# Performance work log

Measured on AMD Instinct MI355X. Metric: run time of the kernel, lower is better.

Reference implementation:

```python
import jax, jax.numpy as jnp
import numpy as np

B, T, V, D, H, A = 256, 512, 50000, 256, 256, 128


def setup_inputs() -> dict:
    key = jax.random.key(0)
    ks = jax.random.split(key, 9)
    x = jax.random.randint(ks[0], (B, T), 0, V, dtype=jnp.int32)
    embed_w = jax.random.uniform(ks[1], (V, D), dtype=jnp.float32)          # random_uniform init, non-trainable
    lstm_kernel = jax.random.normal(ks[2], (D + H, 4 * H), dtype=jnp.float32) * 0.05  # BasicLSTMCell kernel [i,j,f,o]
    lstm_bias = jnp.zeros((4 * H,), jnp.float32)
    w_omega = jax.random.normal(ks[3], (H, A), dtype=jnp.float32)
    b_omega = jax.random.normal(ks[4], (A,), dtype=jnp.float32)
    u_omega = jax.random.normal(ks[5], (A,), dtype=jnp.float32)
    w = jax.random.normal(ks[6], (H, 2), dtype=jnp.float32)
    b = jnp.zeros((2,), jnp.float32)
    return {"x": x, "embed_w": embed_w, "lstm_kernel": lstm_kernel,
            "lstm_bias": lstm_bias, "w_omega": w_omega, "b_omega": b_omega,
            "u_omega": u_omega, "w": w, "b": b}


def _lstm_attention_forward(x, embed_w, lstm_kernel, lstm_bias, w_omega, b_omega, u_omega, w, b):
    Bt, Tt = x.shape
    Hh = lstm_bias.shape[0] // 4
    seq_len = jnp.sum(jnp.sign(x), axis=1)                         # [B] like tf.reduce_sum(tf.sign(x))
    e = embed_w[x]                                                  # [B,T,D] embedding lookup
    # dynamic_rnn semantics: outputs zeroed past seq_len, state frozen
    mask = (jnp.arange(Tt)[:, None] < seq_len[None, :]).astype(e.dtype)  # [T,B]
    xs = (jnp.transpose(e, (1, 0, 2)), mask[:, :, None])            # time-major

    def step(carry, inp):
        c, h = carry
        x_t, m = inp                                                # [B,D], [B,1]
        z = jnp.concatenate([x_t, h], axis=-1) @ lstm_kernel + lstm_bias  # [B,4H]
        i, j, f, o = jnp.split(z, 4, axis=-1)
        c_new = c * jax.nn.sigmoid(f + 1.0) + jax.nn.sigmoid(i) * jnp.tanh(j)  # forget_bias=1.0
        h_new = jnp.tanh(c_new) * jax.nn.sigmoid(o)
        c = jnp.where(m > 0, c_new, c)
        h_out = h_new * m
        h = jnp.where(m > 0, h_new, h)
        return (c, h), h_out

    c0 = jnp.zeros((Bt, Hh), e.dtype)
    h0 = jnp.zeros((Bt, Hh), e.dtype)
    _, outs = jax.lax.scan(step, (c0, h0), xs)                      # [T,B,H]
    outs = jnp.transpose(outs, (1, 0, 2))                           # [B,T,H]

    # additive attention pooling
    value = jnp.tanh(jnp.einsum('bth,ha->bta', outs, w_omega) + b_omega)
    vu = jnp.einsum('bta,a->bt', value, u_omega)
    alphas = jax.nn.softmax(vu, axis=-1)                            # [B,T]
    last = jnp.sum(outs * alphas[..., None], axis=1)                # [B,H]

    logits = last @ w + b                                           # [B,2]
    return jax.nn.softmax(logits)


def reference(x, embed_w, lstm_kernel, lstm_bias, w_omega, b_omega, u_omega, w, b):
    return _lstm_attention_forward(x, embed_w, lstm_kernel, lstm_bias,
                                   w_omega, b_omega, u_omega, w, b)
```

## Files before the change

### kernel.cpp

```cpp
#include <hip/hip_runtime.h>
#include <hip/hip_bf16.h>
#include <cstdint>
#include <cstddef>

typedef _Float16 f16;
typedef _Float16 f16x8 __attribute__((ext_vector_type(8)));
typedef _Float16 f16x4 __attribute__((ext_vector_type(4)));
typedef float f32x4 __attribute__((ext_vector_type(4)));
typedef unsigned long long u64;
typedef unsigned int u32;

#define B_   256
#define T_   512
#define V_   50000
#define D_   256
#define H_   256
#define A_   128
#define N4H  1024

__device__ __forceinline__ float sigmoid_f(float x) {
    return __builtin_amdgcn_rcpf(1.f + __expf(-x));
}
__device__ __forceinline__ float tanh_f(float x) {
    float e = __expf(-2.f * fabsf(x));
    float t = 1.f - 2.f * e * __builtin_amdgcn_rcpf(1.f + e);
    return copysignf(t, x);
}

#define MFMA_A(accv, afragv, bfraga)                                         \
    asm volatile("v_mfma_f32_16x16x32_f16 %0, %1, %2, %0"                    \
                 : "+v"(accv) : "v"(afragv), "a"(bfraga))

#define LGKM_BARRIER()                                                       \
    do {                                                                     \
        asm volatile("s_waitcnt lgkmcnt(0)" ::: "memory");                   \
        __builtin_amdgcn_sched_barrier(0);                                   \
        __builtin_amdgcn_s_barrier();                                        \
        __builtin_amdgcn_sched_barrier(0);                                   \
    } while (0)

__global__ __launch_bounds__(256) void k0_convert(
    const float* __restrict__ lstm_kernel, const float* __restrict__ w_omega,
    f16* __restrict__ WxT, f16* __restrict__ WhT, f16* __restrict__ WomT) {
    int blk = blockIdx.x;
    int tau = threadIdx.x;
    if (blk < N4H) {
        int n = blk;
        WxT[n * 256 + tau] = (f16)lstm_kernel[(size_t)tau * N4H + n];
        WhT[n * 256 + tau] = (f16)lstm_kernel[(size_t)(256 + tau) * N4H + n];
    } else {
        int a = blk - N4H;
        WomT[a * 256 + tau] = (f16)w_omega[(size_t)tau * A_ + a];
    }
}

__global__ __launch_bounds__(256) void k1_seqlen(
    const int* __restrict__ x, int* __restrict__ seqlen) {
    __shared__ int red[256];
    int b = blockIdx.x, tau = threadIdx.x;
    int cnt = (x[b * T_ + tau] != 0) + (x[b * T_ + tau + 256] != 0);
    red[tau] = cnt;
    __syncthreads();
    for (int s = 128; s > 0; s >>= 1) {
        if (tau < s) red[tau] += red[tau + s];
        __syncthreads();
    }
    if (tau == 0) seqlen[b] = red[0];
}

__global__ __launch_bounds__(256) void k2_zx(
    const int* __restrict__ x, const float* __restrict__ embed,
    const f16* __restrict__ WxT, const float* __restrict__ bias,
    f16* __restrict__ Zx, int t0, int Tc) {
    __shared__ __align__(16) f16 A_s[64][264];
    __shared__ __align__(16) f16 B_s[128][72];
    __shared__ int tok_s[64];

    int tau  = threadIdx.x;
    int bm   = blockIdx.x;
    int i0   = bm * 64;
    int wave = tau >> 6, lane = tau & 63;
    int q = lane >> 4, c = lane & 15;

    if (tau < 64) {
        int i  = i0 + tau;
        int bb = i / Tc, tr = i - bb * Tc;
        tok_s[tau] = x[bb * T_ + t0 + tr];
    }
    __syncthreads();

    {
        int r = tau >> 2, quarter = tau & 3;
        const float4* src =
            (const float4*)(embed + (size_t)tok_s[r] * D_ + quarter * 64);
        f16* dst = &A_s[r][quarter * 64];
#pragma unroll
        for (int j = 0; j < 16; j++) {
            float4 v = src[j];
            dst[j * 4 + 0] = (f16)v.x;
            dst[j * 4 + 1] = (f16)v.y;
            dst[j * 4 + 2] = (f16)v.z;
            dst[j * 4 + 3] = (f16)v.w;
        }
    }

    for (int np = 0; np < 8; np++) {
        f32x4 acc[8];
#pragma unroll
        for (int ni = 0; ni < 8; ni++) acc[ni] = (f32x4){0.f, 0.f, 0.f, 0.f};

        for (int kt = 0; kt < 4; kt++) {
            __syncthreads();
            {
                int n = tau >> 1, half = tau & 1;
                const f16x8* src = (const f16x8*)(WxT +
                    (size_t)(np * 128 + n) * 256 + kt * 64 + half * 32);
                f16x8* dst = (f16x8*)&B_s[n][half * 32];
#pragma unroll
                for (int j = 0; j < 4; j++) dst[j] = src[j];
            }
            __syncthreads();
#pragma unroll
            for (int s = 0; s < 2; s++) {
                f16x8 afrag =
                    *(const f16x8*)&A_s[wave * 16 + c][kt * 64 + s * 32 + q * 8];
#pragma unroll
                for (int ni = 0; ni < 8; ni++) {
                    f16x8 bfrag = *(const f16x8*)&B_s[ni * 16 + c][s * 32 + q * 8];
                    acc[ni] = __builtin_amdgcn_mfma_f32_16x16x32_f16(
                        afrag, bfrag, acc[ni], 0, 0, 0);
                }
            }
        }
#pragma unroll
        for (int ni = 0; ni < 8; ni++) {
            int n    = np * 128 + ni * 16 + c;
            int g    = n >> 8, rem = n & 255;
            int half = rem >> 7, colu = rem & 127;
            int np2  = half * 512 + colu * 4 + g;
            float bv = bias[n];
#pragma unroll
            for (int r = 0; r < 4; r++) {
                int row = i0 + wave * 16 + q * 4 + r;
                Zx[(size_t)row * N4H + np2] = (f16)(acc[ni][r] + bv);
            }
        }
    }
}

#define SMEM_BYTES 87040

__device__ __forceinline__ void zx_producer(
    const int* __restrict__ x, const float* __restrict__ embed,
    const f16* __restrict__ WxT, const float* __restrict__ bias,
    f16* __restrict__ Zx, int pb, int t0, int Tc, char* smem) {
    f16 (*Ap_s)[264] = (f16(*)[264])smem;
    f16 (*Bp_s)[72]  = (f16(*)[72])(smem + 67584);
    int* tokp_s      = (int*)(smem + 86016);

    int tau  = threadIdx.x;
    int i0   = pb * 128;
    int wave = tau >> 6, lane = tau & 63;
    int q = lane >> 4, c = lane & 15;

    if (tau < 128) {
        int i  = i0 + tau;
        int bb = i / Tc, tr = i - bb * Tc;
        tokp_s[tau] = x[bb * T_ + t0 + tr];
    }
    __syncthreads();

    {
        int r = tau >> 2, quarter = tau & 3;
        const float4* src =
            (const float4*)(embed + (size_t)tokp_s[r] * D_ + quarter * 64);
        f16* dst = &Ap_s[r][quarter * 64];
#pragma unroll
        for (int j = 0; j < 16; j++) {
            float4 v = src[j];
            dst[j * 4 + 0] = (f16)v.x;
            dst[j * 4 + 1] = (f16)v.y;
            dst[j * 4 + 2] = (f16)v.z;
            dst[j * 4 + 3] = (f16)v.w;
        }
    }

    for (int np = 0; np < 8; np++) {
        f32x4 acc[8];
#pragma unroll
        for (int ni = 0; ni < 8; ni++) acc[ni] = (f32x4){0.f, 0.f, 0.f, 0.f};

        for (int kt = 0; kt < 4; kt++) {
            __syncthreads();
            {
                int n = tau >> 2, qt = tau & 3;
                const f16x8* src = (const f16x8*)(WxT +
                    (size_t)(np * 128 + n) * 256 + kt * 64 + qt * 16);
                f16x8* dst = (f16x8*)&Bp_s[n][qt * 16];
                dst[0] = src[0];
                dst[1] = src[1];
            }
            __syncthreads();
#pragma unroll
            for (int s = 0; s < 2; s++) {
                f16x8 afrag =
                    *(const f16x8*)&Ap_s[wave * 16 + c][kt * 64 + s * 32 + q * 8];
#pragma unroll
                for (int ni = 0; ni < 8; ni++) {
                    f16x8 bfrag = *(const f16x8*)&Bp_s[ni * 16 + c][s * 32 + q * 8];
                    acc[ni] = __builtin_amdgcn_mfma_f32_16x16x32_f16(
                        afrag, bfrag, acc[ni], 0, 0, 0);
                }
            }
        }
#pragma unroll
        for (int ni = 0; ni < 8; ni++) {
            int n     = np * 128 + ni * 16 + c;
            int g     = n >> 8, rem = n & 255;
            int halfn = rem >> 7, colu = rem & 127;
            int np2   = halfn * 512 + colu * 4 + g;
            float bv  = bias[n];
#pragma unroll
            for (int r = 0; r < 4; r++) {
                int row = i0 + wave * 16 + q * 4 + r;
                Zx[(size_t)row * N4H + np2] = (f16)(acc[ni][r] + bv);
            }
        }
    }
}

__device__ __forceinline__ void vu_producer(
    const f16* __restrict__ outs, const f16* __restrict__ WomT,
    const float* __restrict__ b_omega, const float* __restrict__ u_omega,
    float* __restrict__ vuout, int b, int t0v, int Tc, char* smem) {
    f16 (*A_s)[264]   = (f16(*)[264])smem;
    f16 (*val_s)[132] = (f16(*)[132])(smem + 33792);
    float* u_s        = (float*)(smem + 50688);

    int tau  = threadIdx.x;
    int wave = tau >> 6, lane = tau & 63;
    int q = lane >> 4, c = lane & 15;

    if (tau < 128) u_s[tau] = u_omega[tau];
    float bom[8];
#pragma unroll
    for (int ni = 0; ni < 8; ni++) bom[ni] = b_omega[ni * 16 + c];

    int nchap = Tc >> 6;
    for (int ch = 0; ch < nchap; ch++) {
        int t0c = t0v + ch * 64;
        __syncthreads();
        if (tau < 256) {
            int r = tau >> 2, seg = tau & 3;
            const f16x8* src =
                (const f16x8*)(outs + ((size_t)b * T_ + t0c + r) * H_ + seg * 64);
            f16x8* dst = (f16x8*)&A_s[r][seg * 64];
#pragma unroll
            for (int j = 0; j < 8; j++) dst[j] = src[j];
        }
        __syncthreads();
        if (tau < 256) {
            f32x4 acc[8];
#pragma unroll
            for (int ni = 0; ni < 8; ni++) acc[ni] = (f32x4){0.f, 0.f, 0.f, 0.f};
#pragma unroll
            for (int kc = 0; kc < 8; kc++) {
                f16x8 afrag = *(const f16x8*)&A_s[wave * 16 + c][kc * 32 + q * 8];
#pragma unroll
                for (int ni = 0; ni < 8; ni++) {
                    f16x8 bfrag = *(const f16x8*)(WomT +
                        (size_t)(ni * 16 + c) * 256 + kc * 32 + q * 8);
                    acc[ni] = __builtin_amdgcn_mfma_f32_16x16x32_f16(
                        afrag, bfrag, acc[ni], 0, 0, 0);
                }
            }
#pragma unroll
            for (int ni = 0; ni < 8; ni++) {
#pragma unroll
                for (int r = 0; r < 4; r++) {
                    val_s[wave * 16 + q * 4 + r][ni * 16 + c] =
                        (f16)tanh_f(acc[ni][r] + bom[ni]);
                }
            }
        }
        __syncthreads();
        if (tau < 64) {
            float s = 0.f;
#pragma unroll 8
            for (int a = 0; a < 128; a++) s += (float)val_s[tau][a] * u_s[a];
            vuout[(size_t)b * T_ + t0c + tau] = s;
        }
    }
}

__global__ __launch_bounds__(512, 2) void k3_lstm(
    const f16* __restrict__ Zx, const f16* __restrict__ WhT,
    const int* __restrict__ seqlen, f16* __restrict__ outs,
    f16* __restrict__ Hstate, float* __restrict__ Cstate,
    u32* __restrict__ Hex, int t0, int Tc, int first, int last,
    const int* __restrict__ x, const float* __restrict__ embed,
    const f16* __restrict__ WxT, const float* __restrict__ bias,
    f16* __restrict__ ZxNext, int t0n, int npz,
    const f16* __restrict__ WomT, const float* __restrict__ b_omega,
    const float* __restrict__ u_omega, float* __restrict__ vuout, int t0v) {
    __shared__ __align__(16) char smem[SMEM_BYTES];

    if (blockIdx.x >= 32) {
        int pid = blockIdx.x - 32;
        if (pid < npz)
            zx_producer(x, embed, WxT, bias, ZxNext, pid, t0n, Tc, smem);
        else
            vu_producer(outs, WomT, b_omega, u_omega, vuout, pid - npz, t0v,
                        Tc, smem);
        return;
    }

    f16 (*Zx_s)[16][520] = (f16(*)[16][520])smem;
    f16 (*h_s)[16][264]  = (f16(*)[16][264])(smem + 33280);

    int tau  = threadIdx.x;
    int w    = tau >> 6, lane = tau & 63;
    int q = lane >> 4, c = lane & 15;
    int wgid = blockIdx.x;
    int pair = wgid >> 1, half = wgid & 1;
    int b0 = pair * 16;
    int u0 = half * 128, pu0 = (half ^ 1) * 128;
    int u  = u0 + w * 16 + c;
    int col = w * 16 + c;

    u32* hexw_my = Hex + (size_t)wgid * 2 * 2048;
    u32* hexw_pr = Hex + (size_t)(wgid ^ 1) * 2 * 2048;

    f32x4 wha[4][8];
#pragma unroll
    for (int g = 0; g < 4; g++)
#pragma unroll
        for (int s = 0; s < 8; s++) {
            int kc = (s < 4) ? (half * 4 + s) : ((half ^ 1) * 4 + (s - 4));
            f16x8 f = *(const f16x8*)(WhT +
                (size_t)(g * 256 + u0 + w * 16 + c) * 256 + kc * 32 + q * 8);
            f32x4 t = __builtin_bit_cast(f32x4, f);
            asm volatile("" : "=a"(wha[g][s]) : "0"(t));
        }

    int kOwn = half * 128 + q * 8;
    int kPar = (half ^ 1) * 128 + q * 8;

    int p0 = t0 & 1;
    if (first) {
        for (int idx = tau; idx < 2 * 16 * 264; idx += 512)
            ((f16*)h_s)[idx] = (f16)0.f;
    } else {
        for (int idx = tau; idx < 16 * 256; idx += 512) {
            int r = idx >> 8, k = idx & 255;
            h_s[p0][r][k] = Hstate[(b0 + r) * H_ + k];
        }
    }

    float cst[4];
    f16   hprev[4];
    int   sl[4];
#pragma unroll
    for (int r = 0; r < 4; r++) {
        int row = q * 4 + r;
        cst[r]   = first ? 0.f : Cstate[(b0 + row) * H_ + u];
        hprev[r] = first ? (f16)0.f : Hstate[(b0 + row) * H_ + u];
        sl[r]    = seqlen[b0 + row];
    }

    int r_st = tau >> 5;
    int cc   = (tau & 31) * 16;
    const f16* zxrow = Zx + ((size_t)(b0 + r_st) * Tc) * N4H + half * 512 + cc;

    {
        const f16x8* src = (const f16x8*)zxrow;
        f16x8* dst = (f16x8*)&Zx_s[p0][r_st][cc];
        dst[0] = src[0];
        dst[1] = src[1];
    }
    int rr = tau >> 5;
    int uu = (tau & 31) * 4;

    __syncthreads();

    f32x4 accO[4];
#pragma unroll
    for (int g = 0; g < 4; g++) accO[g] = (f32x4){0.f, 0.f, 0.f, 0.f};
#pragma unroll
    for (int kk = 0; kk < 4; kk++) {
        f16x8 afrag = *(const f16x8*)&h_s[p0][c][kOwn + kk * 32];
#pragma unroll
        for (int g = 0; g < 4; g++) MFMA_A(accO[g], afrag, wha[g][kk]);
    }

    u64 vp0 = 0, vp1 = 0;

    for (int tt = 0; tt < Tc; tt++) {
        int t   = t0 + tt;
        int cur = t & 1, nxt = cur ^ 1;

        int tn = (tt + 1 < Tc) ? tt + 1 : tt;
        const f16x8* psrc = (const f16x8*)(zxrow + (size_t)tn * N4H);
        f16x8 z0 = psrc[0];
        f16x8 z1 = psrc[1];

        if (tt > 0) {
            u32 tagp = (u32)(t & 0xffff);
            const u64* pp = (const u64*)&hexw_pr[cur * 2048 + rr * 128 + uu];
            while (((u32)(vp0 >> 16) & 0xffffu) != tagp ||
                   ((u32)(vp0 >> 48)) != tagp ||
                   ((u32)(vp1 >> 16) & 0xffffu) != tagp ||
                   ((u32)(vp1 >> 48)) != tagp) {
                vp0 = __hip_atomic_load(pp + 0, __ATOMIC_RELAXED,
                                        __HIP_MEMORY_SCOPE_AGENT);
                vp1 = __hip_atomic_load(pp + 1, __ATOMIC_RELAXED,
                                        __HIP_MEMORY_SCOPE_AGENT);
            }
            u64 hw = (u64)(vp0 & 0xffff) | (((vp0 >> 32) & 0xffff) << 16) |
                     ((vp1 & 0xffff) << 32) | (((vp1 >> 32) & 0xffff) << 48);
            *(u64*)&h_s[cur][rr][pu0 + uu] = hw;
        }
        LGKM_BARRIER();

#pragma unroll
        for (int kk = 0; kk < 4; kk++) {
            f16x8 afrag = *(const f16x8*)&h_s[cur][c][kPar + kk * 32];
#pragma unroll
            for (int g = 0; g < 4; g++) MFMA_A(accO[g], afrag, wha[g][4 + kk]);
        }

        u32 tag = (u32)((t + 1) & 0xffff);
        f16 ovals[4];
#pragma unroll
        for (int r = 0; r < 4; r++) {
            int row = q * 4 + r;
            f16x4 zv = *(const f16x4*)&Zx_s[cur][row][col * 4];
            float zi = accO[0][r] + (float)zv[0];
            float zj = accO[1][r] + (float)zv[1];
            float zf = accO[2][r] + (float)zv[2];
            float zo = accO[3][r] + (float)zv[3];
            float ig = sigmoid_f(zi);
            float jg = tanh_f(zj);
            float fg = sigmoid_f(zf + 1.f);
            float og = sigmoid_f(zo);
            float cn = cst[r] * fg + ig * jg;
            float hn = tanh_f(cn) * og;
            bool  m  = (t < sl[r]);
            cst[r]   = m ? cn : cst[r];
            f16 hkeep = m ? (f16)hn : hprev[r];
            hprev[r]  = hkeep;
            h_s[nxt][row][u] = hkeep;
            u32 word = (tag << 16) |
                       (u32)(unsigned short)__builtin_bit_cast(short, hkeep);
            __hip_atomic_store(&hexw_my[nxt * 2048 + row * 128 + col], word,
                               __ATOMIC_RELAXED, __HIP_MEMORY_SCOPE_AGENT);
            ovals[r] = m ? (f16)hn : (f16)0.f;
        }

        {
            f16x8* dst = (f16x8*)&Zx_s[nxt][r_st][cc];
            dst[0] = z0;
            dst[1] = z1;
        }

#pragma unroll
        for (int r = 0; r < 4; r++)
            outs[((size_t)(b0 + q * 4 + r) * T_ + t) * H_ + u] = ovals[r];

        {
            const u64* pp2 = (const u64*)&hexw_pr[nxt * 2048 + rr * 128 + uu];
            vp0 = __hip_atomic_load(pp2 + 0, __ATOMIC_RELAXED,
                                    __HIP_MEMORY_SCOPE_AGENT);
            vp1 = __hip_atomic_load(pp2 + 1, __ATOMIC_RELAXED,
                                    __HIP_MEMORY_SCOPE_AGENT);
        }

        LGKM_BARRIER();

#pragma unroll
        for (int g = 0; g < 4; g++) accO[g] = (f32x4){0.f, 0.f, 0.f, 0.f};
#pragma unroll
        for (int kk = 0; kk < 4; kk++) {
            f16x8 afrag = *(const f16x8*)&h_s[nxt][c][kOwn + kk * 32];
#pragma unroll
            for (int g = 0; g < 4; g++) MFMA_A(accO[g], afrag, wha[g][kk]);
        }
    }

    if (!last) {
        int parity = (t0 + Tc) & 1;
        for (int idx = tau; idx < 16 * 128; idx += 512) {
            int r = idx >> 7, k = u0 + (idx & 127);
            Hstate[(b0 + r) * H_ + k] = h_s[parity][r][k];
        }
#pragma unroll
        for (int r = 0; r < 4; r++)
            Cstate[(b0 + q * 4 + r) * H_ + u] = cst[r];
    }
}

__global__ __launch_bounds__(256) void k4_attn(
    const f16* __restrict__ outs, const f16* __restrict__ WomT,
    const float* __restrict__ b_omega, const float* __restrict__ u_omega,
    const float* __restrict__ w, const float* __restrict__ bfin,
    const float* __restrict__ vuin, int tstart, float* __restrict__ out) {
    __shared__ __align__(16) f16 A_s[64][264];
    __shared__ __align__(16) f16 val_s[64][132];
    __shared__ float u_s[128];
    __shared__ float vu_s[512];
    __shared__ float red0[256], red1[256];

    int b = blockIdx.x, tau = threadIdx.x;
    int wave = tau >> 6, lane = tau & 63;
    int q = lane >> 4, c = lane & 15;

    if (tau < 128) u_s[tau] = u_omega[tau];
    float bom[8];
#pragma unroll
    for (int ni = 0; ni < 8; ni++) bom[ni] = b_omega[ni * 16 + c];

    for (int t = tau; t < tstart; t += 256) vu_s[t] = vuin[(size_t)b * T_ + t];

    for (int ch = tstart >> 6; ch < 8; ch++) {
        int t0c = ch * 64;
        __syncthreads();
        {
            int r = tau >> 2, seg = tau & 3;
            const f16x8* src =
                (const f16x8*)(outs + ((size_t)b * T_ + t0c + r) * H_ + seg * 64);
            f16x8* dst = (f16x8*)&A_s[r][seg * 64];
#pragma unroll
            for (int j = 0; j < 8; j++) dst[j] = src[j];
        }
        __syncthreads();

        f32x4 acc[8];
#pragma unroll
        for (int ni = 0; ni < 8; ni++) acc[ni] = (f32x4){0.f, 0.f, 0.f, 0.f};
#pragma unroll
        for (int kc = 0; kc < 8; kc++) {
            f16x8 afrag = *(const f16x8*)&A_s[wave * 16 + c][kc * 32 + q * 8];
#pragma unroll
            for (int ni = 0; ni < 8; ni++) {
                f16x8 bfrag = *(const f16x8*)(WomT +
                    (size_t)(ni * 16 + c) * 256 + kc * 32 + q * 8);
                acc[ni] = __builtin_amdgcn_mfma_f32_16x16x32_f16(
                    afrag, bfrag, acc[ni], 0, 0, 0);
            }
        }
#pragma unroll
        for (int ni = 0; ni < 8; ni++) {
#pragma unroll
            for (int r = 0; r < 4; r++) {
                val_s[wave * 16 + q * 4 + r][ni * 16 + c] =
                    (f16)tanh_f(acc[ni][r] + bom[ni]);
            }
        }
        __syncthreads();
        if (tau < 64) {
            float s = 0.f;
#pragma unroll 8
            for (int a = 0; a < 128; a++) s += (float)val_s[tau][a] * u_s[a];
            vu_s[t0c + tau] = s;
        }
    }
    __syncthreads();

    red0[tau] = fmaxf(vu_s[tau], vu_s[tau + 256]);
    __syncthreads();
    for (int s = 128; s > 0; s >>= 1) {
        if (tau < s) red0[tau] = fmaxf(red0[tau], red0[tau + s]);
        __syncthreads();
    }
    float mx = red0[0];
    __syncthreads();
    float e0 = __expf(vu_s[tau] - mx), e1 = __expf(vu_s[tau + 256] - mx);
    red0[tau] = e0 + e1;
    __syncthreads();
    for (int s = 128; s > 0; s >>= 1) {
        if (tau < s) red0[tau] += red0[tau + s];
        __syncthreads();
    }
    float inv = 1.f / red0[0];
    __syncthreads();
    vu_s[tau]       = e0 * inv;
    vu_s[tau + 256] = e1 * inv;
    __syncthreads();

    float lastv = 0.f;
#pragma unroll 4
    for (int t = 0; t < T_; t++)
        lastv += vu_s[t] * (float)outs[((size_t)b * T_ + t) * H_ + tau];

    red0[tau] = lastv * w[tau * 2 + 0];
    red1[tau] = lastv * w[tau * 2 + 1];
    __syncthreads();
    for (int s = 128; s > 0; s >>= 1) {
        if (tau < s) {
            red0[tau] += red0[tau + s];
            red1[tau] += red1[tau + s];
        }
        __syncthreads();
    }
    if (tau == 0) {
        float l0 = red0[0] + bfin[0], l1 = red1[0] + bfin[1];
        float mm = fmaxf(l0, l1);
        float a0 = __expf(l0 - mm), a1 = __expf(l1 - mm);
        float den = a0 + a1;
        out[b * 2 + 0] = a0 / den;
        out[b * 2 + 1] = a1 / den;
    }
}

extern "C" void kernel_launch(void* const* d_in, const int* in_sizes, int n_in,
                              void* d_out, int out_size, void* d_ws,
                              size_t ws_size, hipStream_t stream) {
    const int*   x           = (const int*)d_in[0];
    const float* embed       = (const float*)d_in[1];
    const float* lstm_kernel = (const float*)d_in[2];
    const float* lstm_bias   = (const float*)d_in[3];
    const float* w_omega     = (const float*)d_in[4];
    const float* b_omega     = (const float*)d_in[5];
    const float* u_omega     = (const float*)d_in[6];
    const float* w           = (const float*)d_in[7];
    const float* bfin        = (const float*)d_in[8];
    float*       out         = (float*)d_out;

    char* ws = (char*)d_ws;
    f16*   WxT    = (f16*)(ws + 0);
    f16*   WhT    = (f16*)(ws + 524288);
    f16*   WomT   = (f16*)(ws + 1048576);
    int*   seqlen = (int*)(ws + 1114112);
    f16*   Hstate = (f16*)(ws + 1115136);
    float* Cstate = (float*)(ws + 1246208);
    u32*   Hex    = (u32*)(ws + 1508352);
    float* vu     = (float*)(ws + 2032640);
    f16*   outs   = (f16*)(ws + 2556928);

    const size_t fixed = 2556928ull + 67108864ull;
    int nch = 1;
    while (nch < 16 && fixed + 2ull * (268435456ull / (size_t)nch) > ws_size)
        nch <<= 1;
    int Tc = T_ / nch;
    size_t chunkB = 268435456ull / (size_t)nch;
    f16* ZxA = (f16*)(ws + fixed);
    f16* ZxB = (f16*)(ws + fixed + chunkB);

    int vuEnable = (Tc % 64 == 0) && (nch >= 2);
    int tstart   = vuEnable ? (nch - 1) * Tc : 0;

    k0_convert<<<1152, 256, 0, stream>>>(lstm_kernel, w_omega, WxT, WhT, WomT);
    k1_seqlen<<<256, 256, 0, stream>>>(x, seqlen);
    k2_zx<<<(B_ * Tc) / 64, 256, 0, stream>>>(x, embed, WxT, lstm_bias, ZxA,
                                              0, Tc);
    for (int chk = 0; chk < nch; chk++) {
        int  t0  = chk * Tc;
        f16* zc  = (chk & 1) ? ZxB : ZxA;
        f16* zn  = (chk & 1) ? ZxA : ZxB;
        int  npz = (chk + 1 < nch) ? (B_ * Tc) / 128 : 0;
        int  nv  = (vuEnable && chk >= 1) ? B_ : 0;
        int  t0n = (chk + 1) * Tc;
        int  t0v = (chk - 1) * Tc;
        k3_lstm<<<32 + npz + nv, 512, 0, stream>>>(
            zc, WhT, seqlen, outs, Hstate, Cstate, Hex, t0, Tc,
            chk == 0 ? 1 : 0, chk == nch - 1 ? 1 : 0,
            x, embed, WxT, lstm_bias, zn, t0n, npz,
            WomT, b_omega, u_omega, vu, t0v);
    }
    k4_attn<<<256, 256, 0, stream>>>(outs, WomT, b_omega, u_omega, w, bfin,
                                     vu, tstart, out);
}
```

Baseline: 1.443 ms.

## Fold first-chunk Zx GEMM into LSTM launch with atomic handoff; widen attention block

Removes the standalone k2_zx launch. The first LSTM launch now also runs extra producer blocks that compute chunk-0 Zx and signal completion through an atomic counter, which the recurrent blocks spin on before starting. The aim is to drop a kernel boundary and overlap setup with the Zx GEMM. The final attention kernel moves to 512 threads and splits the weighted time sum across two thread groups. The cost is a spin-wait that depends on the producer blocks actually getting scheduled while the recurrent blocks wait, which risks stalls or deadlock if residency is limited.

Measured after the change: 1.503 ms. 4.2% more time.

```diff
diff --git a/kernel.cpp b/kernel.cpp
--- a/kernel.cpp
+++ b/kernel.cpp
@@ -41,9 +41,11 @@
 
 __global__ __launch_bounds__(256) void k0_convert(
     const float* __restrict__ lstm_kernel, const float* __restrict__ w_omega,
-    f16* __restrict__ WxT, f16* __restrict__ WhT, f16* __restrict__ WomT) {
+    f16* __restrict__ WxT, f16* __restrict__ WhT, f16* __restrict__ WomT,
+    u32* __restrict__ zdone) {
     int blk = blockIdx.x;
     int tau = threadIdx.x;
+    if (blk == 0 && tau == 0) *zdone = 0;
     if (blk < N4H) {
         int n = blk;
         WxT[n * 256 + tau] = (f16)lstm_kernel[(size_t)tau * N4H + n];
@@ -68,92 +70,12 @@
     if (tau == 0) seqlen[b] = red[0];
 }
 
-__global__ __launch_bounds__(256) void k2_zx(
-    const int* __restrict__ x, const float* __restrict__ embed,
-    const f16* __restrict__ WxT, const float* __restrict__ bias,
-    f16* __restrict__ Zx, int t0, int Tc) {
-    __shared__ __align__(16) f16 A_s[64][264];
-    __shared__ __align__(16) f16 B_s[128][72];
-    __shared__ int tok_s[64];
-
-    int tau  = threadIdx.x;
-    int bm   = blockIdx.x;
-    int i0   = bm * 64;
-    int wave = tau >> 6, lane = tau & 63;
-    int q = lane >> 4, c = lane & 15;
-
-    if (tau < 64) {
-        int i  = i0 + tau;
-        int bb = i / Tc, tr = i - bb * Tc;
-        tok_s[tau] = x[bb * T_ + t0 + tr];
-    }
-    __syncthreads();
-
-    {
-        int r = tau >> 2, quarter = tau & 3;
-        const float4* src =
-            (const float4*)(embed + (size_t)tok_s[r] * D_ + quarter * 64);
-        f16* dst = &A_s[r][quarter * 64];
-#pragma unroll
-        for (int j = 0; j < 16; j++) {
-            float4 v = src[j];
-            dst[j * 4 + 0] = (f16)v.x;
-            dst[j * 4 + 1] = (f16)v.y;
-            dst[j * 4 + 2] = (f16)v.z;
-            dst[j * 4 + 3] = (f16)v.w;
-        }
-    }
-
-    for (int np = 0; np < 8; np++) {
-        f32x4 acc[8];
-#pragma unroll
-        for (int ni = 0; ni < 8; ni++) acc[ni] = (f32x4){0.f, 0.f, 0.f, 0.f};
-
-        for (int kt = 0; kt < 4; kt++) {
-            __syncthreads();
-            {
-                int n = tau >> 1, half = tau & 1;
-                const f16x8* src = (const f16x8*)(WxT +
-                    (size_t)(np * 128 + n) * 256 + kt * 64 + half * 32);
-                f16x8* dst = (f16x8*)&B_s[n][half * 32];
-#pragma unroll
-                for (int j = 0; j < 4; j++) dst[j] = src[j];
-            }
-            __syncthreads();
-#pragma unroll
-            for (int s = 0; s < 2; s++) {
-                f16x8 afrag =
-                    *(const f16x8*)&A_s[wave * 16 + c][kt * 64 + s * 32 + q * 8];
-#pragma unroll
-                for (int ni = 0; ni < 8; ni++) {
-                    f16x8 bfrag = *(const f16x8*)&B_s[ni * 16 + c][s * 32 + q * 8];
-                    acc[ni] = __builtin_amdgcn_mfma_f32_16x16x32_f16(
-                        afrag, bfrag, acc[ni], 0, 0, 0);
-                }
-            }
-        }
-#pragma unroll
-        for (int ni = 0; ni < 8; ni++) {
-            int n    = np * 128 + ni * 16 + c;
-            int g    = n >> 8, rem = n & 255;
-            int half = rem >> 7, colu = rem & 127;
-            int np2  = half * 512 + colu * 4 + g;
-            float bv = bias[n];
-#pragma unroll
-            for (int r = 0; r < 4; r++) {
-                int row = i0 + wave * 16 + q * 4 + r;
-                Zx[(size_t)row * N4H + np2] = (f16)(acc[ni][r] + bv);
-            }
-        }
-    }
-}
-
 #define SMEM_BYTES 87040
 
 __device__ __forceinline__ void zx_producer(
     const int* __restrict__ x, const float* __restrict__ embed,
     const f16* __restrict__ WxT, const float* __restrict__ bias,
-    f16* __restrict__ Zx, int pb, int t0, int Tc, char* smem) {
+    f16* Zx, int pb, int t0, int Tc, char* smem) {
     f16 (*Ap_s)[264] = (f16(*)[264])smem;
     f16 (*Bp_s)[72]  = (f16(*)[72])(smem + 67584);
     int* tokp_s      = (int*)(smem + 86016);
@@ -294,7 +216,7 @@
 }
 
 __global__ __launch_bounds__(512, 2) void k3_lstm(
-    const f16* __restrict__ Zx, const f16* __restrict__ WhT,
+    const f16* Zx, const f16* __restrict__ WhT,
     const int* __restrict__ seqlen, f16* __restrict__ outs,
     f16* __restrict__ Hstate, float* __restrict__ Cstate,
     u32* __restrict__ Hex, int t0, int Tc, int first, int last,
@@ -302,16 +224,24 @@
     const f16* __restrict__ WxT, const float* __restrict__ bias,
     f16* __restrict__ ZxNext, int t0n, int npz,
     const f16* __restrict__ WomT, const float* __restrict__ b_omega,
-    const float* __restrict__ u_omega, float* __restrict__ vuout, int t0v) {
+    const float* __restrict__ u_omega, float* __restrict__ vuout, int t0v,
+    f16* ZxCurW, int nz0, u32* __restrict__ zdone) {
     __shared__ __align__(16) char smem[SMEM_BYTES];
 
     if (blockIdx.x >= 32) {
         int pid = blockIdx.x - 32;
-        if (pid < npz)
-            zx_producer(x, embed, WxT, bias, ZxNext, pid, t0n, Tc, smem);
-        else
-            vu_producer(outs, WomT, b_omega, u_omega, vuout, pid - npz, t0v,
-                        Tc, smem);
+        if (pid < nz0) {
+            zx_producer(x, embed, WxT, bias, ZxCurW, pid, t0, Tc, smem);
+            __syncthreads();
+            if (threadIdx.x == 0)
+                __hip_atomic_fetch_add(zdone, 1u, __ATOMIC_RELEASE,
+                                       __HIP_MEMORY_SCOPE_AGENT);
+        } else if (pid - nz0 < npz) {
+            zx_producer(x, embed, WxT, bias, ZxNext, pid - nz0, t0n, Tc, smem);
+        } else {
+            vu_producer(outs, WomT, b_omega, u_omega, vuout, pid - nz0 - npz,
+                        t0v, Tc, smem);
+        }
         return;
     }
 
@@ -366,6 +296,14 @@
         cst[r]   = first ? 0.f : Cstate[(b0 + row) * H_ + u];
         hprev[r] = first ? (f16)0.f : Hstate[(b0 + row) * H_ + u];
         sl[r]    = seqlen[b0 + row];
+    }
+
+    if (first) {
+        if (tau == 0) {
+            while (__hip_atomic_load(zdone, __ATOMIC_ACQUIRE,
+                                     __HIP_MEMORY_SCOPE_AGENT) < (u32)nz0) {}
+        }
+        __syncthreads();
     }
 
     int r_st = tau >> 5;
@@ -499,7 +437,7 @@
     }
 }
 
-__global__ __launch_bounds__(256) void k4_attn(
+__global__ __launch_bounds__(512) void k4_attn(
     const f16* __restrict__ outs, const f16* __restrict__ WomT,
     const float* __restrict__ b_omega, const float* __restrict__ u_omega,
     const float* __restrict__ w, const float* __restrict__ bfin,
@@ -508,7 +446,7 @@
     __shared__ __align__(16) f16 val_s[64][132];
     __shared__ float u_s[128];
     __shared__ float vu_s[512];
-    __shared__ float red0[256], red1[256];
+    __shared__ float red0[512], red1[512];
 
     int b = blockIdx.x, tau = threadIdx.x;
     int wave = tau >> 6, lane = tau & 63;
@@ -519,12 +457,12 @@
 #pragma unroll
     for (int ni = 0; ni < 8; ni++) bom[ni] = b_omega[ni * 16 + c];
 
-    for (int t = tau; t < tstart; t += 256) vu_s[t] = vuin[(size_t)b * T_ + t];
+    for (int t = tau; t < tstart; t += 512) vu_s[t] = vuin[(size_t)b * T_ + t];
 
     for (int ch = tstart >> 6; ch < 8; ch++) {
         int t0c = ch * 64;
         __syncthreads();
-        {
+        if (tau < 256) {
             int r = tau >> 2, seg = tau & 3;
             const f16x8* src =
                 (const f16x8*)(outs + ((size_t)b * T_ + t0c + r) * H_ + seg * 64);
@@ -533,27 +471,28 @@
             for (int j = 0; j < 8; j++) dst[j] = src[j];
         }
         __syncthreads();
-
-        f32x4 acc[8];
-#pragma unroll
-        for (int ni = 0; ni < 8; ni++) acc[ni] = (f32x4){0.f, 0.f, 0.f, 0.f};
-#pragma unroll
-        for (int kc = 0; kc < 8; kc++) {
-            f16x8 afrag = *(const f16x8*)&A_s[wave * 16 + c][kc * 32 + q * 8];
+        if (tau < 256) {
+            f32x4 acc[8];
+#pragma unroll
+            for (int ni = 0; ni < 8; ni++) acc[ni] = (f32x4){0.f, 0.f, 0.f, 0.f};
+#pragma unroll
+            for (int kc = 0; kc < 8; kc++) {
+                f16x8 afrag = *(const f16x8*)&A_s[wave * 16 + c][kc * 32 + q * 8];
+#pragma unroll
+                for (int ni = 0; ni < 8; ni++) {
+                    f16x8 bfrag = *(const f16x8*)(WomT +
+                        (size_t)(ni * 16 + c) * 256 + kc * 32 + q * 8);
+                    acc[ni] = __builtin_amdgcn_mfma_f32_16x16x32_f16(
+                        afrag, bfrag, acc[ni], 0, 0, 0);
+                }
+            }
 #pragma unroll
             for (int ni = 0; ni < 8; ni++) {
-                f16x8 bfrag = *(const f16x8*)(WomT +
-                    (size_t)(ni * 16 + c) * 256 + kc * 32 + q * 8);
-                acc[ni] = __builtin_amdgcn_mfma_f32_16x16x32_f16(
-                    afrag, bfrag, acc[ni], 0, 0, 0);
-            }
-        }
-#pragma unroll
-        for (int ni = 0; ni < 8; ni++) {
-#pragma unroll
-            for (int r = 0; r < 4; r++) {
-                val_s[wave * 16 + q * 4 + r][ni * 16 + c] =
-                    (f16)tanh_f(acc[ni][r] + bom[ni]);
+#pragma unroll
+                for (int r = 0; r < 4; r++) {
+                    val_s[wave * 16 + q * 4 + r][ni * 16 + c] =
+                        (f16)tanh_f(acc[ni][r] + bom[ni]);
+                }
             }
         }
         __syncthreads();
@@ -566,36 +505,44 @@
     }
     __syncthreads();
 
-    red0[tau] = fmaxf(vu_s[tau], vu_s[tau + 256]);
-    __syncthreads();
-    for (int s = 128; s > 0; s >>= 1) {
+    red0[tau] = vu_s[tau];
+    __syncthreads();
+    for (int s = 256; s > 0; s >>= 1) {
         if (tau < s) red0[tau] = fmaxf(red0[tau], red0[tau + s]);
         __syncthreads();
     }
     float mx = red0[0];
     __syncthreads();
-    float e0 = __expf(vu_s[tau] - mx), e1 = __expf(vu_s[tau + 256] - mx);
-    red0[tau] = e0 + e1;
-    __syncthreads();
-    for (int s = 128; s > 0; s >>= 1) {
+    float e = __expf(vu_s[tau] - mx);
+    red0[tau] = e;
+    __syncthreads();
+    for (int s = 256; s > 0; s >>= 1) {
         if (tau < s) red0[tau] += red0[tau + s];
         __syncthreads();
     }
     float inv = 1.f / red0[0];
     __syncthreads();
-    vu_s[tau]       = e0 * inv;
-    vu_s[tau + 256] = e1 * inv;
-    __syncthreads();
-
+    vu_s[tau] = e * inv;
+    __syncthreads();
+
+    int h = tau & 255, tg = tau >> 8;
     float lastv = 0.f;
+    {
+        const f16* orow = outs + ((size_t)b * T_ + tg * 256) * H_ + h;
+        const float* al = &vu_s[tg * 256];
 #pragma unroll 4
-    for (int t = 0; t < T_; t++)
-        lastv += vu_s[t] * (float)outs[((size_t)b * T_ + t) * H_ + tau];
-
-    red0[tau] = lastv * w[tau * 2 + 0];
-    red1[tau] = lastv * w[tau * 2 + 1];
-    __syncthreads();
-    for (int s = 128; s > 0; s >>= 1) {
+        for (int t = 0; t < 256; t++)
+            lastv += al[t] * (float)orow[(size_t)t * H_];
+    }
+    red0[tau] = lastv;
+    __syncthreads();
+    float lsum = (tau < 256) ? red0[tau] + red0[tau + 256] : 0.f;
+    __syncthreads();
+
+    red0[tau] = (tau < 256) ? lsum * w[h * 2 + 0] : 0.f;
+    red1[tau] = (tau < 256) ? lsum * w[h * 2 + 1] : 0.f;
+    __syncthreads();
+    for (int s = 256; s > 0; s >>= 1) {
         if (tau < s) {
             red0[tau] += red0[tau + s];
             red1[tau] += red1[tau + s];
@@ -634,10 +581,11 @@
     f16*   Hstate = (f16*)(ws + 1115136);
     float* Cstate = (float*)(ws + 1246208);
     u32*   Hex    = (u32*)(ws + 1508352);
-    float* vu     = (float*)(ws + 2032640);
-    f16*   outs   = (f16*)(ws + 2556928);
-
-    const size_t fixed = 2556928ull + 67108864ull;
+    u32*   zdone  = (u32*)(ws + 2032640);
+    float* vu     = (float*)(ws + 2033664);
+    f16*   outs   = (f16*)(ws + 2557952);
+
+    const size_t fixed = 2557952ull + 67108864ull;
     int nch = 1;
     while (nch < 16 && fixed + 2ull * (268435456ull / (size_t)nch) > ws_size)
         nch <<= 1;
@@ -648,25 +596,27 @@
 
     int vuEnable = (Tc % 64 == 0) && (nch >= 2);
     int tstart   = vuEnable ? (nch - 1) * Tc : 0;
-
-    k0_convert<<<1152, 256, 0, stream>>>(lstm_kernel, w_omega, WxT, WhT, WomT);
+    int nz0all   = (B_ * Tc) / 128;
+
+    k0_convert<<<1152, 256, 0, stream>>>(lstm_kernel, w_omega, WxT, WhT, WomT,
+                                         zdone);
     k1_seqlen<<<256, 256, 0, stream>>>(x, seqlen);
-    k2_zx<<<(B_ * Tc) / 64, 256, 0, stream>>>(x, embed, WxT, lstm_bias, ZxA,
-                                              0, Tc);
     for (int chk = 0; chk < nch; chk++) {
         int  t0  = chk * Tc;
         f16* zc  = (chk & 1) ? ZxB : ZxA;
         f16* zn  = (chk & 1) ? ZxA : ZxB;
+        int  nzp = (chk == 0) ? nz0all : 0;
         int  npz = (chk + 1 < nch) ? (B_ * Tc) / 128 : 0;
         int  nv  = (vuEnable && chk >= 1) ? B_ : 0;
         int  t0n = (chk + 1) * Tc;
         int  t0v = (chk - 1) * Tc;
-        k3_lstm<<<32 + npz + nv, 512, 0, stream>>>(
+        k3_lstm<<<32 + nzp + npz + nv, 512, 0, stream>>>(
             zc, WhT, seqlen, outs, Hstate, Cstate, Hex, t0, Tc,
             chk == 0 ? 1 : 0, chk == nch - 1 ? 1 : 0,
             x, embed, WxT, lstm_bias, zn, t0n, npz,
-            WomT, b_omega, u_omega, vu, t0v);
-    }
-    k4_attn<<<256, 256, 0, stream>>>(outs, WomT, b_omega, u_omega, w, bfin,
+            WomT, b_omega, u_omega, vu, t0v,
+            zc, nzp, zdone);
+    }
+    k4_attn<<<256, 512, 0, stream>>>(outs, WomT, b_omega, u_omega, w, bfin,
                                      vu, tstart, out);
 }
```
